# Kernel optimization log

Hardware: AMD Instinct MI355X
Metric: run time of the kernel (lower is better)

Reference implementation:

```python
import jax, jax.numpy as jnp
import numpy as np

BN_EPS = 1e-3  # Keras BatchNormalization default epsilon

def _conv2d_same(x, w, b):
    # x: NHWC, w: HWIO (kh,kw,2,1)
    y = jax.lax.conv_general_dilated(x, w, window_strides=(1, 1), padding='SAME',
                                     dimension_numbers=('NHWC', 'HWIO', 'NHWC'))
    return y + b

def _zpool(t):
    # concat([max, avg], axis=-1) over channel axis -> last dim = 2
    return jnp.concatenate([jnp.max(t, axis=-1, keepdims=True),
                            jnp.mean(t, axis=-1, keepdims=True)], axis=-1)

def _att_map(t2, w, b, g, beta, mean, var):
    y = _conv2d_same(t2, w, b)
    y = (y - mean) * jax.lax.rsqrt(var + BN_EPS) * g + beta  # inference BN
    return jax.nn.sigmoid(y)

def setup_inputs() -> dict:
    key = jax.random.key(0)
    ks = jax.random.split(key, 8)
    B, H, W, C, K, RR = 32, 56, 56, 256, 7, 8
    d = {}
    d['x'] = jax.random.normal(ks[0], (B, H, W, C), dtype=jnp.float32)
    for i, kk in zip((1, 2, 3), ks[1:4]):
        d[f'conv{i}_w'] = jax.random.normal(kk, (K, K, 2, 1), dtype=jnp.float32) * 0.1
        d[f'conv{i}_b'] = jnp.zeros((1,), dtype=jnp.float32)
        d[f'bn{i}_g'] = jnp.ones((1,), dtype=jnp.float32)
        d[f'bn{i}_b'] = jnp.zeros((1,), dtype=jnp.float32)
        d[f'bn{i}_m'] = jnp.zeros((1,), dtype=jnp.float32)
        d[f'bn{i}_v'] = jnp.ones((1,), dtype=jnp.float32)
    Ch = C // RR
    d['se_w1'] = jax.random.normal(ks[4], (C, Ch), dtype=jnp.float32) * (2.0 / C) ** 0.5
    d['se_b1'] = jnp.zeros((Ch,), dtype=jnp.float32)
    d['se_w2'] = jax.random.normal(ks[5], (Ch, C), dtype=jnp.float32) * 0.05
    d['se_b2'] = jnp.zeros((C,), dtype=jnp.float32)
    return d

def reference(x, conv1_w, conv1_b, bn1_g, bn1_b, bn1_m, bn1_v,
              conv2_w, conv2_b, bn2_g, bn2_b, bn2_m, bn2_v,
              conv3_w, conv3_b, bn3_g, bn3_b, bn3_m, bn3_v,
              se_w1, se_b1, se_w2, se_b2):
    # Branch 1 (H-axis): permute (B,H,W,C)->(B,H,C,W), pool over W
    th1 = jnp.transpose(x, (0, 1, 3, 2))
    a1 = _att_map(_zpool(th1), conv1_w, conv1_b, bn1_g, bn1_b, bn1_m, bn1_v)
    br1 = jnp.transpose(th1 * a1, (0, 1, 3, 2))
    # Branch 2 (W-axis): permute (B,H,W,C)->(B,C,W,H), pool over H
    th2 = jnp.transpose(x, (0, 3, 2, 1))
    a2 = _att_map(_zpool(th2), conv2_w, conv2_b, bn2_g, bn2_b, bn2_m, bn2_v)
    br2 = jnp.transpose(th2 * a2, (0, 3, 2, 1))
    # Branch 3 (identity): pool over C
    a3 = _att_map(_zpool(x), conv3_w, conv3_b, bn3_g, bn3_b, bn3_m, bn3_v)
    br3 = x * a3
    # TriSE1: Add branches, then SE channel gating
    s = br1 + br2 + br3
    gap = jnp.mean(s, axis=(1, 2), keepdims=True)            # (B,1,1,C)
    h = jax.nn.relu(jnp.einsum('bijc,cd->bijd', gap, se_w1) + se_b1)
    cw = jax.nn.sigmoid(jnp.einsum('bijd,dc->bijc', h, se_w2) + se_b2)
    return s * cw
```

## Files before the change

### kernel.cpp

```cpp
#include <hip/hip_runtime.h>
#include <math.h>

namespace {
constexpr int B = 32, H = 56, W = 56, C = 256;
constexpr int HW  = H * W;
constexpr int WC  = W * C;
constexpr int HC  = H * C;
constexpr int HWC = H * W * C;
constexpr int CH  = 32;
constexpr float BN_EPS = 1e-3f;

using f4v = __attribute__((ext_vector_type(4))) float;

__device__ __forceinline__ float sigmoidf_(float v) { return 1.0f / (1.0f + expf(-v)); }

__device__ __forceinline__ void nt_store_float4(float* p, const float4& o) {
    union { float4 s; f4v v; } u;
    u.s = o;
    __builtin_nontemporal_store(u.v, (f4v*)p);
}
}

__global__ __launch_bounds__(256)
void pool_all_kernel(const float* __restrict__ x,
                     float* __restrict__ pmax1, float* __restrict__ pavg1,
                     float* __restrict__ pmax2, float* __restrict__ pavg2,
                     float* __restrict__ pmax3, float* __restrict__ pavg3) {
    const int t = threadIdx.x;

    if (blockIdx.x < B * H) {
        const int lane = t & 63, sub = t >> 6;
        const int c4 = lane * 4;
        __shared__ float smx[4][256];
        __shared__ float ssm[4][256];
        const int b = blockIdx.x / H, h = blockIdx.x % H;
        const float* xp = x + (size_t)b * HWC + (size_t)h * WC;
        float4 mx = make_float4(-INFINITY, -INFINITY, -INFINITY, -INFINITY);
        float4 sm = make_float4(0.f, 0.f, 0.f, 0.f);
        for (int wq = 0; wq < 14; ++wq) {
            const int w = wq * 4 + sub;
            const float4 v = *(const float4*)(xp + w * C + c4);
            mx.x = fmaxf(mx.x, v.x); mx.y = fmaxf(mx.y, v.y);
            mx.z = fmaxf(mx.z, v.z); mx.w = fmaxf(mx.w, v.w);
            sm.x += v.x; sm.y += v.y; sm.z += v.z; sm.w += v.w;
            float m3 = fmaxf(fmaxf(v.x, v.y), fmaxf(v.z, v.w));
            float s3 = v.x + v.y + v.z + v.w;
            #pragma unroll
            for (int off = 32; off > 0; off >>= 1) {
                m3 = fmaxf(m3, __shfl_down(m3, off));
                s3 += __shfl_down(s3, off);
            }
            if (lane == 0) {
                pmax3[b * HW + h * W + w] = m3;
                pavg3[b * HW + h * W + w] = s3 * (1.0f / C);
            }
        }
        *(float4*)&smx[sub][c4] = mx;
        *(float4*)&ssm[sub][c4] = sm;
        __syncthreads();
        const float m = fmaxf(fmaxf(smx[0][t], smx[1][t]), fmaxf(smx[2][t], smx[3][t]));
        const float s = ssm[0][t] + ssm[1][t] + ssm[2][t] + ssm[3][t];
        pmax1[b * HC + h * C + t] = m;
        pavg1[b * HC + h * C + t] = s * (1.0f / W);
    } else {
        const int tt = blockIdx.x - B * H;
        const int b = tt / 14, wq = tt % 14;
        const int w = wq * 4 + (t >> 6);
        const int c4 = (t & 63) * 4;
        const float* xp = x + (size_t)b * HWC + (size_t)w * C + c4;
        float4 mx = make_float4(-INFINITY, -INFINITY, -INFINITY, -INFINITY);
        float4 sm = make_float4(0.f, 0.f, 0.f, 0.f);
        #pragma unroll 8
        for (int h = 0; h < H; ++h) {
            const float4 v = *(const float4*)(xp + (size_t)h * WC);
            mx.x = fmaxf(mx.x, v.x); mx.y = fmaxf(mx.y, v.y);
            mx.z = fmaxf(mx.z, v.z); mx.w = fmaxf(mx.w, v.w);
            sm.x += v.x; sm.y += v.y; sm.z += v.z; sm.w += v.w;
        }
        const int oi = b * WC + w * C + c4;
        *(float4*)(pmax2 + oi) = mx;
        float4 av;
        av.x = sm.x * (1.0f / H); av.y = sm.y * (1.0f / H);
        av.z = sm.z * (1.0f / H); av.w = sm.w * (1.0f / H);
        *(float4*)(pavg2 + oi) = av;
    }
}

__global__ __launch_bounds__(256)
void conv_all_kernel(const float* __restrict__ pmax1, const float* __restrict__ pavg1,
                     const float* __restrict__ pmax2, const float* __restrict__ pavg2,
                     const float* __restrict__ pmax3, const float* __restrict__ pavg3,
                     const float* __restrict__ c1w, const float* __restrict__ c1b,
                     const float* __restrict__ g1,  const float* __restrict__ be1,
                     const float* __restrict__ m1,  const float* __restrict__ v1,
                     const float* __restrict__ c2w, const float* __restrict__ c2b,
                     const float* __restrict__ g2,  const float* __restrict__ be2,
                     const float* __restrict__ m2,  const float* __restrict__ v2,
                     const float* __restrict__ c3w, const float* __restrict__ c3b,
                     const float* __restrict__ g3,  const float* __restrict__ be3,
                     const float* __restrict__ m3,  const float* __restrict__ v3,
                     float* __restrict__ a1, float* __restrict__ a2t, float* __restrict__ a3) {
    const int t = threadIdx.x;
    __shared__ float wg[98];
    __shared__ float sm[7][264];
    __shared__ float sa[7][264];

    if (blockIdx.x < B * H) {
        if (t < 98) wg[t] = c1w[t];
        const int b = blockIdx.x / H, h = blockIdx.x % H;
        const float* bm = pmax1 + b * HC;
        const float* ba = pavg1 + b * HC;
        #pragma unroll
        for (int ky = 0; ky < 7; ++ky) {
            const int hy = h + ky - 3;
            const bool val = (hy >= 0 && hy < H);
            const int hyc = min(max(hy, 0), H - 1);
            const float lm = bm[hyc * C + t];
            const float la = ba[hyc * C + t];
            sm[ky][t + 3] = val ? lm : 0.f;
            sa[ky][t + 3] = val ? la : 0.f;
            if (t < 3) { sm[ky][t] = 0.f; sa[ky][t] = 0.f; sm[ky][261 - t] = 0.f; sa[ky][261 - t] = 0.f; }
        }
        __syncthreads();
        const float A  = rsqrtf(v1[0] + BN_EPS) * g1[0];
        const float Bc = (c1b[0] - m1[0]) * A + be1[0];
        float acc = 0.f;
        #pragma unroll
        for (int ky = 0; ky < 7; ++ky)
            #pragma unroll
            for (int kx = 0; kx < 7; ++kx)
                acc += sm[ky][t + kx] * wg[ky * 14 + kx * 2] + sa[ky][t + kx] * wg[ky * 14 + kx * 2 + 1];
        a1[b * HC + h * C + t] = sigmoidf_(acc * A + Bc);
    } else if (blockIdx.x < 2 * B * H) {
        if (t < 98) wg[t] = c2w[t];
        const int tt = blockIdx.x - B * H;
        const int b = tt / W, w = tt % W;
        #pragma unroll
        for (int kx = 0; kx < 7; ++kx) {
            const int wx = w + kx - 3;
            const bool val = (wx >= 0 && wx < W);
            const int wxc = min(max(wx, 0), W - 1);
            const float lm = pmax2[b * WC + wxc * C + t];
            const float la = pavg2[b * WC + wxc * C + t];
            sm[kx][t + 3] = val ? lm : 0.f;
            sa[kx][t + 3] = val ? la : 0.f;
            if (t < 3) { sm[kx][t] = 0.f; sa[kx][t] = 0.f; sm[kx][261 - t] = 0.f; sa[kx][261 - t] = 0.f; }
        }
        __syncthreads();
        const float A  = rsqrtf(v2[0] + BN_EPS) * g2[0];
        const float Bc = (c2b[0] - m2[0]) * A + be2[0];
        float acc = 0.f;
        #pragma unroll
        for (int kx = 0; kx < 7; ++kx)
            #pragma unroll
            for (int ky = 0; ky < 7; ++ky)
                acc += sm[kx][t + ky] * wg[ky * 14 + kx * 2] + sa[kx][t + ky] * wg[ky * 14 + kx * 2 + 1];
        a2t[b * WC + w * C + t] = sigmoidf_(acc * A + Bc);
    } else {
        if (t < 98) wg[t] = c3w[t];
        __syncthreads();
        const int gid = (blockIdx.x - 2 * B * H) * 256 + t;
        const int b = gid / HW;
        const int hw = gid % HW;
        const int h = hw / W, w = hw % W;
        const float A  = rsqrtf(v3[0] + BN_EPS) * g3[0];
        const float Bc = (c3b[0] - m3[0]) * A + be3[0];
        float acc = 0.f;
        const float* bm = pmax3 + b * HW;
        const float* ba = pavg3 + b * HW;
        #pragma unroll
        for (int ky = 0; ky < 7; ++ky) {
            const int hy = h + ky - 3;
            if (hy < 0 || hy >= H) continue;
            #pragma unroll
            for (int kx = 0; kx < 7; ++kx) {
                const int wx = w + kx - 3;
                if (wx < 0 || wx >= W) continue;
                acc += bm[hy * W + wx] * wg[ky * 14 + kx * 2] + ba[hy * W + wx] * wg[ky * 14 + kx * 2 + 1];
            }
        }
        a3[b * HW + hw] = sigmoidf_(acc * A + Bc);
    }
}

__global__ __launch_bounds__(256)
void gap_row_kernel(const float* __restrict__ x, const float* __restrict__ a3,
                    float* __restrict__ gpart) {
    const int b = blockIdx.x / H, h = blockIdx.x % H;
    const int t = threadIdx.x;
    const int lane = t & 63, sub = t >> 6;
    const int c4 = lane * 4;
    const float* xp = x + (size_t)b * HWC + (size_t)h * WC;
    float4 acc = make_float4(0.f, 0.f, 0.f, 0.f);
    for (int wq = 0; wq < 14; ++wq) {
        const int w = wq * 4 + sub;
        const float4 xv = *(const float4*)(xp + w * C + c4);
        const float a3v = a3[b * HW + h * W + w];
        acc.x += xv.x * a3v;
        acc.y += xv.y * a3v;
        acc.z += xv.z * a3v;
        acc.w += xv.w * a3v;
    }
    __shared__ float sacc[4][256];
    *(float4*)&sacc[sub][c4] = acc;
    __syncthreads();
    gpart[(size_t)blockIdx.x * C + t] = sacc[0][t] + sacc[1][t] + sacc[2][t] + sacc[3][t];
}

__global__ __launch_bounds__(256)
void se_kernel(const float* __restrict__ gpart,
               const float* __restrict__ a1,  const float* __restrict__ pavg1,
               const float* __restrict__ a2t, const float* __restrict__ pavg2,
               const float* __restrict__ w1, const float* __restrict__ b1,
               const float* __restrict__ w2, const float* __restrict__ b2,
               float* __restrict__ cw) {
    const int b = blockIdx.x;
    const int t = threadIdx.x;
    __shared__ float gs[C];
    __shared__ float hs[CH];
    float s1 = 0.f, s2 = 0.f, s3 = 0.f;
    for (int r = 0; r < H; ++r) {
        s1 += a1 [b * HC + r * C + t] * pavg1[b * HC + r * C + t];
        s2 += a2t[b * WC + r * C + t] * pavg2[b * WC + r * C + t];
        s3 += gpart[(size_t)(b * H + r) * C + t];
    }
    gs[t] = (s1 + s2) * (1.0f / 56.0f) + s3 * (1.0f / (float)HW);
    __syncthreads();
    if (t < CH) {
        float a = b1[t];
        for (int c = 0; c < C; ++c) a += gs[c] * w1[c * CH + t];
        hs[t] = fmaxf(a, 0.f);
    }
    __syncthreads();
    float a = b2[t];
    #pragma unroll
    for (int d = 0; d < CH; ++d) a += hs[d] * w2[d * C + t];
    cw[b * C + t] = sigmoidf_(a);
}

__global__ __launch_bounds__(256)
void out_row_kernel(const float* __restrict__ x, const float* __restrict__ a1,
                    const float* __restrict__ a2t, const float* __restrict__ a3,
                    const float* __restrict__ cw, float* __restrict__ out) {
    const int b = blockIdx.x / H, h = blockIdx.x % H;
    const int t = threadIdx.x;
    const int lane = t & 63, sub = t >> 6;
    const int c4 = lane * 4;
    const float* xp  = x   + (size_t)b * HWC + (size_t)h * WC;
    const float* a2b = a2t + (size_t)b * WC;
    float*       op  = out + (size_t)b * HWC + (size_t)h * WC;
    const float4 a1v = *(const float4*)(a1 + b * HC + h * C + c4);
    const float4 cwv = *(const float4*)(cw + b * C + c4);
    for (int wq = 0; wq < 14; ++wq) {
        const int w = wq * 4 + sub;
        const float4 xv  = *(const float4*)(xp  + w * C + c4);
        const float4 a2v = *(const float4*)(a2b + w * C + c4);
        const float a3v  = a3[b * HW + h * W + w];
        float4 o;
        o.x = xv.x * (a1v.x + a2v.x + a3v) * cwv.x;
        o.y = xv.y * (a1v.y + a2v.y + a3v) * cwv.y;
        o.z = xv.z * (a1v.z + a2v.z + a3v) * cwv.z;
        o.w = xv.w * (a1v.w + a2v.w + a3v) * cwv.w;
        nt_store_float4(op + w * C + c4, o);
    }
}

extern "C" void kernel_launch(void* const* d_in, const int* in_sizes, int n_in,
                              void* d_out, int out_size, void* d_ws, size_t ws_size,
                              hipStream_t stream) {
    const float* x   = (const float*)d_in[0];
    const float* c1w = (const float*)d_in[1];  const float* c1b = (const float*)d_in[2];
    const float* g1  = (const float*)d_in[3];  const float* be1 = (const float*)d_in[4];
    const float* m1  = (const float*)d_in[5];  const float* v1  = (const float*)d_in[6];
    const float* c2w = (const float*)d_in[7];  const float* c2b = (const float*)d_in[8];
    const float* g2  = (const float*)d_in[9];  const float* be2 = (const float*)d_in[10];
    const float* m2  = (const float*)d_in[11]; const float* v2  = (const float*)d_in[12];
    const float* c3w = (const float*)d_in[13]; const float* c3b = (const float*)d_in[14];
    const float* g3  = (const float*)d_in[15]; const float* be3 = (const float*)d_in[16];
    const float* m3  = (const float*)d_in[17]; const float* v3  = (const float*)d_in[18];
    const float* sw1 = (const float*)d_in[19]; const float* sb1 = (const float*)d_in[20];
    const float* sw2 = (const float*)d_in[21]; const float* sb2 = (const float*)d_in[22];

    float* ws = (float*)d_ws;
    float* pmax1 = ws;
    float* pavg1 = pmax1 + (size_t)B * HC;
    float* pmax2 = pavg1 + (size_t)B * HC;
    float* pavg2 = pmax2 + (size_t)B * WC;
    float* pmax3 = pavg2 + (size_t)B * WC;
    float* pavg3 = pmax3 + (size_t)B * HW;
    float* a1    = pavg3 + (size_t)B * HW;
    float* a2t   = a1    + (size_t)B * HC;
    float* a3    = a2t   + (size_t)B * WC;
    float* gpart = a3    + (size_t)B * HW;
    float* cwv   = gpart + (size_t)B * H * C;

    pool_all_kernel<<<B * H + B * 14, 256, 0, stream>>>(x, pmax1, pavg1, pmax2, pavg2, pmax3, pavg3);
    conv_all_kernel<<<2 * B * H + (B * HW) / 256, 256, 0, stream>>>(
        pmax1, pavg1, pmax2, pavg2, pmax3, pavg3,
        c1w, c1b, g1, be1, m1, v1,
        c2w, c2b, g2, be2, m2, v2,
        c3w, c3b, g3, be3, m3, v3,
        a1, a2t, a3);
    gap_row_kernel<<<B * H, 256, 0, stream>>>(x, a3, gpart);
    se_kernel<<<B, 256, 0, stream>>>(gpart, a1, pavg1, a2t, pavg2, sw1, sb1, sw2, sb2, cwv);
    out_row_kernel<<<B * H, 256, 0, stream>>>(x, a1, a2t, a3, cwv, (float*)d_out);
}
```

Before: 299.4 us.

## Batch loads for MLP, split H-pooling across waves, tile branch-3 conv in LDS

```diff
diff --git a/kernel.cpp b/kernel.cpp
--- a/kernel.cpp
+++ b/kernel.cpp
@@ -27,30 +27,36 @@
                      float* __restrict__ pmax2, float* __restrict__ pavg2,
                      float* __restrict__ pmax3, float* __restrict__ pavg3) {
     const int t = threadIdx.x;
+    const int lane = t & 63, sub = t >> 6;
+    const int c4 = lane * 4;
+    __shared__ float smx[4][256];
+    __shared__ float ssm[4][256];
 
     if (blockIdx.x < B * H) {
-        const int lane = t & 63, sub = t >> 6;
-        const int c4 = lane * 4;
-        __shared__ float smx[4][256];
-        __shared__ float ssm[4][256];
         const int b = blockIdx.x / H, h = blockIdx.x % H;
-        const float* xp = x + (size_t)b * HWC + (size_t)h * WC;
-        float4 mx = make_float4(-INFINITY, -INFINITY, -INFINITY, -INFINITY);
-        float4 sm = make_float4(0.f, 0.f, 0.f, 0.f);
+        const float* xp = x + (size_t)b * HWC + (size_t)h * WC + c4;
+        float4 v[14];
+        #pragma unroll
+        for (int wq = 0; wq < 14; ++wq)
+            v[wq] = *(const float4*)(xp + (wq * 4 + sub) * C);
+        float4 mx = v[0], sm = v[0];
+        #pragma unroll
+        for (int wq = 1; wq < 14; ++wq) {
+            mx.x = fmaxf(mx.x, v[wq].x); mx.y = fmaxf(mx.y, v[wq].y);
+            mx.z = fmaxf(mx.z, v[wq].z); mx.w = fmaxf(mx.w, v[wq].w);
+            sm.x += v[wq].x; sm.y += v[wq].y; sm.z += v[wq].z; sm.w += v[wq].w;
+        }
+        #pragma unroll
         for (int wq = 0; wq < 14; ++wq) {
-            const int w = wq * 4 + sub;
-            const float4 v = *(const float4*)(xp + w * C + c4);
-            mx.x = fmaxf(mx.x, v.x); mx.y = fmaxf(mx.y, v.y);
-            mx.z = fmaxf(mx.z, v.z); mx.w = fmaxf(mx.w, v.w);
-            sm.x += v.x; sm.y += v.y; sm.z += v.z; sm.w += v.w;
-            float m3 = fmaxf(fmaxf(v.x, v.y), fmaxf(v.z, v.w));
-            float s3 = v.x + v.y + v.z + v.w;
+            float m3 = fmaxf(fmaxf(v[wq].x, v[wq].y), fmaxf(v[wq].z, v[wq].w));
+            float s3 = v[wq].x + v[wq].y + v[wq].z + v[wq].w;
             #pragma unroll
             for (int off = 32; off > 0; off >>= 1) {
                 m3 = fmaxf(m3, __shfl_down(m3, off));
                 s3 += __shfl_down(s3, off);
             }
             if (lane == 0) {
+                const int w = wq * 4 + sub;
                 pmax3[b * HW + h * W + w] = m3;
                 pavg3[b * HW + h * W + w] = s3 * (1.0f / C);
             }
@@ -64,25 +70,26 @@
         pavg1[b * HC + h * C + t] = s * (1.0f / W);
     } else {
         const int tt = blockIdx.x - B * H;
-        const int b = tt / 14, wq = tt % 14;
-        const int w = wq * 4 + (t >> 6);
-        const int c4 = (t & 63) * 4;
+        const int b = tt / W, w = tt % W;
         const float* xp = x + (size_t)b * HWC + (size_t)w * C + c4;
-        float4 mx = make_float4(-INFINITY, -INFINITY, -INFINITY, -INFINITY);
-        float4 sm = make_float4(0.f, 0.f, 0.f, 0.f);
-        #pragma unroll 8
-        for (int h = 0; h < H; ++h) {
-            const float4 v = *(const float4*)(xp + (size_t)h * WC);
-            mx.x = fmaxf(mx.x, v.x); mx.y = fmaxf(mx.y, v.y);
-            mx.z = fmaxf(mx.z, v.z); mx.w = fmaxf(mx.w, v.w);
-            sm.x += v.x; sm.y += v.y; sm.z += v.z; sm.w += v.w;
-        }
-        const int oi = b * WC + w * C + c4;
-        *(float4*)(pmax2 + oi) = mx;
-        float4 av;
-        av.x = sm.x * (1.0f / H); av.y = sm.y * (1.0f / H);
-        av.z = sm.z * (1.0f / H); av.w = sm.w * (1.0f / H);
-        *(float4*)(pavg2 + oi) = av;
+        float4 v[14];
+        #pragma unroll
+        for (int i = 0; i < 14; ++i)
+            v[i] = *(const float4*)(xp + (size_t)(i * 4 + sub) * WC);
+        float4 mx = v[0], sm = v[0];
+        #pragma unroll
+        for (int i = 1; i < 14; ++i) {
+            mx.x = fmaxf(mx.x, v[i].x); mx.y = fmaxf(mx.y, v[i].y);
+            mx.z = fmaxf(mx.z, v[i].z); mx.w = fmaxf(mx.w, v[i].w);
+            sm.x += v[i].x; sm.y += v[i].y; sm.z += v[i].z; sm.w += v[i].w;
+        }
+        *(float4*)&smx[sub][c4] = mx;
+        *(float4*)&ssm[sub][c4] = sm;
+        __syncthreads();
+        const float m = fmaxf(fmaxf(smx[0][t], smx[1][t]), fmaxf(smx[2][t], smx[3][t]));
+        const float s = ssm[0][t] + ssm[1][t] + ssm[2][t] + ssm[3][t];
+        pmax2[(size_t)b * WC + w * C + t] = m;
+        pavg2[(size_t)b * WC + w * C + t] = s * (1.0f / H);
     }
 }
 
@@ -102,14 +109,13 @@
                      float* __restrict__ a1, float* __restrict__ a2t, float* __restrict__ a3) {
     const int t = threadIdx.x;
     __shared__ float wg[98];
-    __shared__ float sm[7][264];
-    __shared__ float sa[7][264];
+    __shared__ float2 sp[7][264];
 
     if (blockIdx.x < B * H) {
         if (t < 98) wg[t] = c1w[t];
         const int b = blockIdx.x / H, h = blockIdx.x % H;
-        const float* bm = pmax1 + b * HC;
-        const float* ba = pavg1 + b * HC;
+        const float* bm = pmax1 + (size_t)b * HC;
+        const float* ba = pavg1 + (size_t)b * HC;
         #pragma unroll
         for (int ky = 0; ky < 7; ++ky) {
             const int hy = h + ky - 3;
@@ -117,9 +123,8 @@
             const int hyc = min(max(hy, 0), H - 1);
             const float lm = bm[hyc * C + t];
             const float la = ba[hyc * C + t];
-            sm[ky][t + 3] = val ? lm : 0.f;
-            sa[ky][t + 3] = val ? la : 0.f;
-            if (t < 3) { sm[ky][t] = 0.f; sa[ky][t] = 0.f; sm[ky][261 - t] = 0.f; sa[ky][261 - t] = 0.f; }
+            sp[ky][t + 3] = val ? make_float2(lm, la) : make_float2(0.f, 0.f);
+            if (t < 3) { sp[ky][t] = make_float2(0.f, 0.f); sp[ky][261 - t] = make_float2(0.f, 0.f); }
         }
         __syncthreads();
         const float A  = rsqrtf(v1[0] + BN_EPS) * g1[0];
@@ -128,8 +133,10 @@
         #pragma unroll
         for (int ky = 0; ky < 7; ++ky)
             #pragma unroll
-            for (int kx = 0; kx < 7; ++kx)
-                acc += sm[ky][t + kx] * wg[ky * 14 + kx * 2] + sa[ky][t + kx] * wg[ky * 14 + kx * 2 + 1];
+            for (int kx = 0; kx < 7; ++kx) {
+                const float2 p = sp[ky][t + kx];
+                acc += p.x * wg[ky * 14 + kx * 2] + p.y * wg[ky * 14 + kx * 2 + 1];
+            }
         a1[b * HC + h * C + t] = sigmoidf_(acc * A + Bc);
     } else if (blockIdx.x < 2 * B * H) {
         if (t < 98) wg[t] = c2w[t];
@@ -140,11 +147,10 @@
             const int wx = w + kx - 3;
             const bool val = (wx >= 0 && wx < W);
             const int wxc = min(max(wx, 0), W - 1);
-            const float lm = pmax2[b * WC + wxc * C + t];
-            const float la = pavg2[b * WC + wxc * C + t];
-            sm[kx][t + 3] = val ? lm : 0.f;
-            sa[kx][t + 3] = val ? la : 0.f;
-            if (t < 3) { sm[kx][t] = 0.f; sa[kx][t] = 0.f; sm[kx][261 - t] = 0.f; sa[kx][261 - t] = 0.f; }
+            const float lm = pmax2[(size_t)b * WC + wxc * C + t];
+            const float la = pavg2[(size_t)b * WC + wxc * C + t];
+            sp[kx][t + 3] = val ? make_float2(lm, la) : make_float2(0.f, 0.f);
+            if (t < 3) { sp[kx][t] = make_float2(0.f, 0.f); sp[kx][261 - t] = make_float2(0.f, 0.f); }
         }
         __syncthreads();
         const float A  = rsqrtf(v2[0] + BN_EPS) * g2[0];
@@ -153,33 +159,42 @@
         #pragma unroll
         for (int kx = 0; kx < 7; ++kx)
             #pragma unroll
-            for (int ky = 0; ky < 7; ++ky)
-                acc += sm[kx][t + ky] * wg[ky * 14 + kx * 2] + sa[kx][t + ky] * wg[ky * 14 + kx * 2 + 1];
-        a2t[b * WC + w * C + t] = sigmoidf_(acc * A + Bc);
+            for (int ky = 0; ky < 7; ++ky) {
+                const float2 p = sp[kx][t + ky];
+                acc += p.x * wg[ky * 14 + kx * 2] + p.y * wg[ky * 14 + kx * 2 + 1];
+            }
+        a2t[(size_t)b * WC + w * C + t] = sigmoidf_(acc * A + Bc);
     } else {
         if (t < 98) wg[t] = c3w[t];
-        __syncthreads();
-        const int gid = (blockIdx.x - 2 * B * H) * 256 + t;
-        const int b = gid / HW;
-        const int hw = gid % HW;
-        const int h = hw / W, w = hw % W;
-        const float A  = rsqrtf(v3[0] + BN_EPS) * g3[0];
-        const float Bc = (c3b[0] - m3[0]) * A + be3[0];
-        float acc = 0.f;
-        const float* bm = pmax3 + b * HW;
-        const float* ba = pavg3 + b * HW;
-        #pragma unroll
-        for (int ky = 0; ky < 7; ++ky) {
-            const int hy = h + ky - 3;
-            if (hy < 0 || hy >= H) continue;
+        float2 (*sp3)[66] = (float2(*)[66])sp;
+        const int tt = blockIdx.x - 2 * B * H;
+        const int b = tt / 14, h0 = (tt % 14) * 4;
+        const float* bm = pmax3 + (size_t)b * HW;
+        const float* ba = pavg3 + (size_t)b * HW;
+        for (int idx = t; idx < 10 * 62; idx += 256) {
+            const int r = idx / 62, col = idx % 62;
+            const int hh = h0 + r - 3, ww = col - 3;
+            const bool val = (hh >= 0 && hh < H && ww >= 0 && ww < W);
+            const int hs = min(max(hh, 0), H - 1), wsx = min(max(ww, 0), W - 1);
+            const float pm = bm[hs * W + wsx];
+            const float pa = ba[hs * W + wsx];
+            sp3[r][col] = val ? make_float2(pm, pa) : make_float2(0.f, 0.f);
+        }
+        __syncthreads();
+        if (t < 224) {
+            const int r = t / 56, w = t % 56;
+            const float A  = rsqrtf(v3[0] + BN_EPS) * g3[0];
+            const float Bc = (c3b[0] - m3[0]) * A + be3[0];
+            float acc = 0.f;
             #pragma unroll
-            for (int kx = 0; kx < 7; ++kx) {
-                const int wx = w + kx - 3;
-                if (wx < 0 || wx >= W) continue;
-                acc += bm[hy * W + wx] * wg[ky * 14 + kx * 2] + ba[hy * W + wx] * wg[ky * 14 + kx * 2 + 1];
-            }
-        }
-        a3[b * HW + hw] = sigmoidf_(acc * A + Bc);
+            for (int ky = 0; ky < 7; ++ky)
+                #pragma unroll
+                for (int kx = 0; kx < 7; ++kx) {
+                    const float2 p = sp3[r + ky][w + kx];
+                    acc += p.x * wg[ky * 14 + kx * 2] + p.y * wg[ky * 14 + kx * 2 + 1];
+                }
+            a3[b * HW + (h0 + r) * W + w] = sigmoidf_(acc * A + Bc);
+        }
     }
 }
 
@@ -190,16 +205,21 @@
     const int t = threadIdx.x;
     const int lane = t & 63, sub = t >> 6;
     const int c4 = lane * 4;
-    const float* xp = x + (size_t)b * HWC + (size_t)h * WC;
+    const float* xp = x + (size_t)b * HWC + (size_t)h * WC + c4;
+    const float* ap = a3 + b * HW + h * W + sub;
+    float4 v[14]; float av[14];
+    #pragma unroll
+    for (int wq = 0; wq < 14; ++wq) {
+        v[wq]  = *(const float4*)(xp + (wq * 4 + sub) * C);
+        av[wq] = ap[wq * 4];
+    }
     float4 acc = make_float4(0.f, 0.f, 0.f, 0.f);
+    #pragma unroll
     for (int wq = 0; wq < 14; ++wq) {
-        const int w = wq * 4 + sub;
-        const float4 xv = *(const float4*)(xp + w * C + c4);
-        const float a3v = a3[b * HW + h * W + w];
-        acc.x += xv.x * a3v;
-        acc.y += xv.y * a3v;
-        acc.z += xv.z * a3v;
-        acc.w += xv.w * a3v;
+        acc.x += v[wq].x * av[wq];
+        acc.y += v[wq].y * av[wq];
+        acc.z += v[wq].z * av[wq];
+        acc.w += v[wq].w * av[wq];
     }
     __shared__ float sacc[4][256];
     *(float4*)&sacc[sub][c4] = acc;
@@ -217,18 +237,37 @@
     const int b = blockIdx.x;
     const int t = threadIdx.x;
     __shared__ float gs[C];
+    __shared__ float part[8][33];
     __shared__ float hs[CH];
+    const float* pa = a1    + (size_t)b * HC + t;
+    const float* pv = pavg1 + (size_t)b * HC + t;
+    const float* qa = a2t   + (size_t)b * WC + t;
+    const float* qv = pavg2 + (size_t)b * WC + t;
+    const float* gp = gpart + (size_t)b * H * C + t;
     float s1 = 0.f, s2 = 0.f, s3 = 0.f;
+    #pragma unroll 8
     for (int r = 0; r < H; ++r) {
-        s1 += a1 [b * HC + r * C + t] * pavg1[b * HC + r * C + t];
-        s2 += a2t[b * WC + r * C + t] * pavg2[b * WC + r * C + t];
-        s3 += gpart[(size_t)(b * H + r) * C + t];
+        s1 += pa[r * C] * pv[r * C];
+        s2 += qa[r * C] * qv[r * C];
+        s3 += gp[r * C];
     }
     gs[t] = (s1 + s2) * (1.0f / 56.0f) + s3 * (1.0f / (float)HW);
+    __syncthreads();
+    {
+        const int d = t & 31, j = t >> 5;
+        float a = 0.f;
+        #pragma unroll
+        for (int i = 0; i < 32; ++i) {
+            const int c = j * 32 + i;
+            a += gs[c] * w1[c * CH + d];
+        }
+        part[j][d] = a;
+    }
     __syncthreads();
     if (t < CH) {
         float a = b1[t];
-        for (int c = 0; c < C; ++c) a += gs[c] * w1[c * CH + t];
+        #pragma unroll
+        for (int j = 0; j < 8; ++j) a += part[j][t];
         hs[t] = fmaxf(a, 0.f);
     }
     __syncthreads();
@@ -246,22 +285,24 @@
     const int t = threadIdx.x;
     const int lane = t & 63, sub = t >> 6;
     const int c4 = lane * 4;
-    const float* xp  = x   + (size_t)b * HWC + (size_t)h * WC;
-    const float* a2b = a2t + (size_t)b * WC;
-    float*       op  = out + (size_t)b * HWC + (size_t)h * WC;
+    const float* xp  = x   + (size_t)b * HWC + (size_t)h * WC + c4;
+    const float* a2b = a2t + (size_t)b * WC + c4;
+    float*       op  = out + (size_t)b * HWC + (size_t)h * WC + c4;
     const float4 a1v = *(const float4*)(a1 + b * HC + h * C + c4);
     const float4 cwv = *(const float4*)(cw + b * C + c4);
+    const float* ap = a3 + b * HW + h * W + sub;
+    #pragma unroll
     for (int wq = 0; wq < 14; ++wq) {
-        const int w = wq * 4 + sub;
-        const float4 xv  = *(const float4*)(xp  + w * C + c4);
-        const float4 a2v = *(const float4*)(a2b + w * C + c4);
-        const float a3v  = a3[b * HW + h * W + w];
+        const int off = (wq * 4 + sub) * C;
+        const float4 xv  = *(const float4*)(xp  + off);
+        const float4 a2v = *(const float4*)(a2b + off);
+        const float a3v  = ap[wq * 4];
         float4 o;
         o.x = xv.x * (a1v.x + a2v.x + a3v) * cwv.x;
         o.y = xv.y * (a1v.y + a2v.y + a3v) * cwv.y;
         o.z = xv.z * (a1v.z + a2v.z + a3v) * cwv.z;
         o.w = xv.w * (a1v.w + a2v.w + a3v) * cwv.w;
-        nt_store_float4(op + w * C + c4, o);
+        nt_store_float4(op + off, o);
     }
 }
 
@@ -294,8 +335,8 @@
     float* gpart = a3    + (size_t)B * HW;
     float* cwv   = gpart + (size_t)B * H * C;
 
-    pool_all_kernel<<<B * H + B * 14, 256, 0, stream>>>(x, pmax1, pavg1, pmax2, pavg2, pmax3, pavg3);
-    conv_all_kernel<<<2 * B * H + (B * HW) / 256, 256, 0, stream>>>(
+    pool_all_kernel<<<B * H + B * W, 256, 0, stream>>>(x, pmax1, pavg1, pmax2, pavg2, pmax3, pavg3);
+    conv_all_kernel<<<2 * B * H + B * 14, 256, 0, stream>>>(
         pmax1, pavg1, pmax2, pavg2, pmax3, pavg3,
         c1w, c1b, g1, be1, m1, v1,
         c2w, c2b, g2, be2, m2, v2,
```

New measurement: 291.4 us. 1.03x faster.
